# Kernel tuning notes

Measured on AMD Instinct MI355X. Metric: run time of the kernel, lower is better.

Reference implementation:

```python
import jax, jax.numpy as jnp
import numpy as np

# Module hyperparameters (from init_kwargs)
H, F = 8, 32            # num_heads, attention_filters
RY, RX = 3, 3           # spatial_radius
PH, PW = 2 * RY + 1, 2 * RX + 1
S = PH * PW             # patch_size = 49
HF = H * F


def setup_inputs() -> dict:
    key = jax.random.key(0)
    ks = jax.random.split(key, 6)
    B, Y, X, C = 4, 64, 64, 256
    x = jax.random.normal(ks[0], (B, Y, X, C), jnp.float32)
    # 1x1 conv kernels == dense matrices over the channel dim (no bias)
    Wq = jax.random.normal(ks[1], (C, HF), jnp.float32) / np.sqrt(C)
    Wk = jax.random.normal(ks[2], (C, HF), jnp.float32) / np.sqrt(C)
    Wv = jax.random.normal(ks[3], (C, HF), jnp.float32) / np.sqrt(C)
    Wo = jax.random.normal(ks[4], (HF, C), jnp.float32) / np.sqrt(HF)
    pos_emb = jax.random.normal(ks[5], (S, HF), jnp.float32) * 0.02
    return {"x": x, "Wq": Wq, "Wk": Wk, "Wv": Wv, "Wo": Wo, "pos_emb": pos_emb}


def reference(x, Wq, Wk, Wv, Wo, pos_emb):
    B, Y, X, C = x.shape
    dtype = x.dtype
    # 1x1 conv projections
    Q = x @ Wq                       # (B,Y,X,HF)
    K = x @ Wk
    V = x @ Wv
    # clipped patch centers (borders reuse interior patches)
    cy = jnp.clip(jnp.arange(Y), RY, Y - RY - 1)   # (Y,)
    cx = jnp.clip(jnp.arange(X), RX, X - RX - 1)   # (X,)
    # query relative-position indices within its patch
    qy = jnp.arange(Y) - cy + RY
    qx = jnp.arange(X) - cx + RX
    qidx = qy[:, None] * PW + qx[None, :]          # (Y,X) in [0,S)
    Q = Q + pos_emb[qidx]                          # add query pos embedding (HF)
    Q = Q.reshape(B, Y, X, H, F)
    K = K.reshape(B, Y, X, H, F)
    V = V.reshape(B, Y, X, H, F)
    cy_g, cx_g = jnp.meshgrid(cy, cx, indexing="ij")  # (Y,X)
    scale = jnp.asarray(1.0 / np.sqrt(F), dtype)
    NEG = jnp.asarray(-1e9, dtype)
    m = jnp.full((B, Y, X, H, 1), NEG, dtype)      # running max
    l = jnp.zeros((B, Y, X, H, 1), dtype)          # running sum-exp
    acc = jnp.zeros((B, Y, X, H, F), dtype)        # running value accumulator
    dy_vec = np.arange(-RY, RY + 1)                # within-chunk offsets ('col' mode)
    for dx in range(-RX, RX + 1):                  # chunk loop over columns (7 chunks)
        ny = jnp.clip(cy_g[None, :, :] + dy_vec[:, None, None], 0, Y - 1)  # (PH,Y,X)
        nx = jnp.clip(cx_g[None, :, :] + dx, 0, X - 1)                     # (1,Y,X)
        nx = jnp.broadcast_to(nx, ny.shape)
        sidx = (dy_vec + RY) * PW + (dx + RX)      # (PH,) relative-pos indices
        # gather neighbor K/V: (B,PH,Y,X,H,F)
        Kc = K[:, ny, nx] + pos_emb[sidx].reshape(PH, 1, 1, H, F)
        Vc = V[:, ny, nx]
        sc = jnp.einsum("byxhf,bsyxhf->byxhs", Q, Kc) * scale  # (B,Y,X,H,PH)
        new_m = jnp.maximum(m, sc.max(axis=-1, keepdims=True))
        alpha = jnp.exp(m - new_m)
        p = jnp.exp(sc - new_m)
        l = l * alpha + p.sum(axis=-1, keepdims=True)
        acc = acc * alpha + jnp.einsum("byxhs,bsyxhf->byxhf", p, Vc)
        m = new_m
    out = (acc / (l + 1e-8)).reshape(B, Y, X, HF) @ Wo
    return out
```

## Files before the change

kernel.cpp:

```cpp
#include <hip/hip_runtime.h>
#include <hip/hip_bf16.h>

static constexpr int NPOS = 4 * 64 * 64;
static constexpr int CD   = 256;
#define QSCALE (0.17677669529663687f * 1.4426950408889634f)

typedef __attribute__((ext_vector_type(8))) short bf16x8;
typedef __attribute__((ext_vector_type(4))) float f32x4;

__device__ __forceinline__ unsigned short bfbits(float f) {
    union { __hip_bfloat16 h; unsigned short u; } cv;
    cv.h = __float2bfloat16(f);
    return cv.u;
}
__device__ __forceinline__ unsigned int packbf2(float lo, float hi) {
    union { __hip_bfloat162 h; unsigned int u; } cv;
    cv.h.x = __float2bfloat16(lo);
    cv.h.y = __float2bfloat16(hi);
    return cv.u;
}
__device__ __forceinline__ uint4 pack8(float4 a, float4 b) {
    uint4 u;
    u.x = packbf2(a.x, a.y); u.y = packbf2(a.z, a.w);
    u.z = packbf2(b.x, b.y); u.w = packbf2(b.z, b.w);
    return u;
}
template<int CTRL>
__device__ __forceinline__ float dpp_mov(float v) {
    return __int_as_float(
        __builtin_amdgcn_update_dpp(0, __float_as_int(v), CTRL, 0xF, 0xF, true));
}
template<int IMM>
__device__ __forceinline__ float swz(float v) {
    return __int_as_float(__builtin_amdgcn_ds_swizzle(__float_as_int(v), IMM));
}
__device__ __forceinline__ void async16(void* lds, const void* g) {
    __builtin_amdgcn_global_load_lds(
        (const __attribute__((address_space(1))) unsigned int*)g,
        (__attribute__((address_space(3))) unsigned int*)lds, 16, 0, 0);
}

__global__ __launch_bounds__(256) void convert_kernel(
    const float* __restrict__ Wq, const float* __restrict__ Wk,
    const float* __restrict__ Wv, const float* __restrict__ Wo,
    const float* __restrict__ pe,
    __hip_bfloat16* __restrict__ Wfrag,
    __hip_bfloat16* __restrict__ pebf,
    __hip_bfloat16* __restrict__ Wofrag)
{
    int t = blockIdx.x * 256 + threadIdx.x;
    if (t < 24576) {
        int L = t & 63, ng = (t >> 6) & 7, s = (t >> 9) & 7, T = t >> 12;
        int mat = T >> 1;
        const float* src = (mat == 0) ? Wq : (mat == 1) ? Wk : Wv;
        int ncol  = (T & 1) * 128 + ng * 16 + (L & 15);
        int kbase = s * 32 + (L >> 4) * 8;
        __hip_bfloat16* dst = Wfrag + ((size_t)((T * 8 + s) * 8 + ng) * 64 + L) * 8;
#pragma unroll
        for (int j = 0; j < 8; ++j)
            dst[j] = __float2bfloat16(src[(kbase + j) * 256 + ncol]);
    } else if (t < 26624) {
        int u = t - 24576;
        int L = u & 63, Tn = (u >> 6) & 3, h = u >> 8;
        int s = Tn * 16 + (L & 15);
        int kbase = (L >> 4) * 8;
        __hip_bfloat16* dst = pebf + ((size_t)((h * 4 + Tn) * 64 + L)) * 8;
#pragma unroll
        for (int j = 0; j < 8; ++j) {
            float v = (s < 49) ? pe[s * 256 + h * 32 + kbase + j] * QSCALE : 0.f;
            dst[j] = __float2bfloat16(v);
        }
    } else if (t < 34816) {
        int u = t - 26624;
        int L = u & 63, ng = (u >> 6) & 7, s = (u >> 9) & 7, T = (u >> 12) & 1;
        int ncol  = T * 128 + ng * 16 + (L & 15);
        int kbase = s * 32 + (L >> 4) * 8;
        __hip_bfloat16* dst = Wofrag + ((size_t)((T * 8 + s) * 8 + ng) * 64 + L) * 8;
#pragma unroll
        for (int j = 0; j < 8; ++j)
            dst[j] = __float2bfloat16(Wo[(kbase + j) * 256 + ncol]);
    }
}

__global__ __launch_bounds__(256, 4) void qkv_mfma(
    const float* __restrict__ x,
    const __hip_bfloat16* __restrict__ Wfrag,
    const float* __restrict__ pe,
    unsigned short* __restrict__ QA,
    unsigned short* __restrict__ Kd,
    unsigned short* __restrict__ Vt)
{
    __shared__ __align__(16) unsigned short smem[256 * 68];
    short* As0 = (short*)smem;
    short* As1 = As0 + 2048;
    const int t = threadIdx.x;
    const int rowbase = blockIdx.x * 64;
    const int g = blockIdx.y;
    const int L = t & 63;
    const int wave = t >> 6;
    const int quad = L >> 4, lrow = L & 15;
    const int T = g * 2 + (wave >> 1);
    const int ngb = (wave & 1) * 4;

    f32x4 acc[4][4];
#pragma unroll
    for (int i = 0; i < 4; ++i)
#pragma unroll
        for (int j = 0; j < 4; ++j) acc[i][j] = (f32x4){0.f, 0.f, 0.f, 0.f};

    const float* xsrc = x + (size_t)(rowbase + (t >> 2)) * CD + (t & 3) * 8;

    float4 f0 = ((const float4*)xsrc)[0];
    float4 f1 = ((const float4*)xsrc)[1];
    ((uint4*)As0)[t] = pack8(f0, f1);
    f0 = ((const float4*)(xsrc + 32))[0];
    f1 = ((const float4*)(xsrc + 32))[1];
    __syncthreads();

#pragma unroll
    for (int s = 0; s < 8; ++s) {
        bf16x8 bfr[4];
#pragma unroll
        for (int j = 0; j < 4; ++j)
            bfr[j] = *(const bf16x8*)(Wfrag +
                      ((size_t)((T * 8 + s) * 8 + ngb + j) * 64 + L) * 8);
        if (s < 7) {
            ((uint4*)((s & 1) ? As0 : As1))[t] = pack8(f0, f1);
            if (s < 6) {
                f0 = ((const float4*)(xsrc + (s + 2) * 32))[0];
                f1 = ((const float4*)(xsrc + (s + 2) * 32))[1];
            }
        }
        const short* Ab = (s & 1) ? As1 : As0;
#pragma unroll
        for (int i = 0; i < 4; ++i) {
            bf16x8 af = *(const bf16x8*)(Ab + (i * 16 + lrow) * 32 + quad * 8);
#pragma unroll
            for (int j = 0; j < 4; ++j)
                acc[i][j] = __builtin_amdgcn_mfma_f32_16x16x32_bf16(af, bfr[j], acc[i][j], 0, 0, 0);
        }
        __syncthreads();
    }

    if (g == 0) {
#pragma unroll
        for (int i = 0; i < 4; ++i)
#pragma unroll
            for (int r = 0; r < 4; ++r) {
                int row = rowbase + i * 16 + quad * 4 + r;
                int yy = (row >> 6) & 63, xx = row & 63;
                int cy = min(max(yy, 3), 60), cx = min(max(xx, 3), 60);
                int qidx = (yy - cy + 3) * 7 + (xx - cx + 3);
#pragma unroll
                for (int j = 0; j < 4; ++j) {
                    int c = wave * 64 + j * 16 + lrow;
                    QA[(size_t)row * CD + c] = bfbits(acc[i][j][r] + pe[qidx * 256 + c]);
                }
            }
    } else if (g == 1) {
#pragma unroll
        for (int i = 0; i < 4; ++i)
#pragma unroll
            for (int r = 0; r < 4; ++r) {
                int row = rowbase + i * 16 + quad * 4 + r;
#pragma unroll
                for (int j = 0; j < 4; ++j) {
                    int c = wave * 64 + j * 16 + lrow;
                    Kd[(size_t)row * CD + c] = bfbits(acc[i][j][r] * QSCALE);
                }
            }
    } else {
        unsigned short* vt = smem;
#pragma unroll
        for (int i = 0; i < 4; ++i)
#pragma unroll
            for (int j = 0; j < 4; ++j) {
                int c = wave * 64 + j * 16 + lrow;
                int row0 = i * 16 + quad * 4;
                *(unsigned int*)&vt[c * 68 + row0] =
                    (unsigned int)bfbits(acc[i][j][0]) | ((unsigned int)bfbits(acc[i][j][1]) << 16);
                *(unsigned int*)&vt[c * 68 + row0 + 2] =
                    (unsigned int)bfbits(acc[i][j][2]) | ((unsigned int)bfbits(acc[i][j][3]) << 16);
            }
        __syncthreads();
        const int grp = t >> 4, lig = t & 15;
        const int row_off = lig * 4;
#pragma unroll
        for (int pass = 0; pass < 16; ++pass) {
            int c = pass * 16 + grp;
            *(ushort4*)(Vt + (size_t)c * 16384 + rowbase + row_off) =
                *(const ushort4*)&vt[c * 68 + row_off];
        }
    }
}

__global__ __launch_bounds__(256) void attn_mfma(
    unsigned short* QA,
    const unsigned short* __restrict__ Kd,
    const unsigned short* __restrict__ Vt,
    const __hip_bfloat16* __restrict__ pebf)
{
    __shared__ float qpes[4][16 * 64];
    __shared__ __align__(16) unsigned short ps[4][16 * 40];
    const int t = threadIdx.x, w = t >> 6, L = t & 63;
    const int lrow = L & 15, quad = L >> 4;
    const int id = blockIdx.x * 4 + w;
    const int tile = id >> 3, h = id & 7;
    const int pos0 = tile * 16;
    const int x0 = pos0 & 63;
    const int yy = (pos0 >> 6) & 63, bb = pos0 >> 12;
    const int cy = min(max(yy, 3), 60);

    int cxr[4];
#pragma unroll
    for (int r = 0; r < 4; ++r)
        cxr[r] = min(max(x0 + quad * 4 + r, 3), 60) - x0 + 5;

    const int kc0 = min(max(x0 - 8 + lrow, 0), 63);
    const int kc1 = min(max(x0 + 8 + lrow, 0), 63);

    const bf16x8 qa = *(const bf16x8*)(QA + (size_t)(pos0 + lrow) * 256 + h * 32 + quad * 8);

    float* qp = qpes[w];
    const f32x4 zero = {0.f, 0.f, 0.f, 0.f};
#pragma unroll
    for (int Tn = 0; Tn < 4; ++Tn) {
        bf16x8 bp = *(const bf16x8*)(pebf + ((size_t)((h * 4 + Tn) * 64 + L)) * 8);
        f32x4 c = __builtin_amdgcn_mfma_f32_16x16x32_bf16(qa, bp, zero, 0, 0, 0);
#pragma unroll
        for (int r = 0; r < 4; ++r)
            qp[(quad * 4 + r) * 64 + Tn * 16 + lrow] = c[r];
    }
    __builtin_amdgcn_s_waitcnt(0xc07f);

    float lacc[4] = {0.f, 0.f, 0.f, 0.f};
    f32x4 o0 = zero, o1 = zero;
    unsigned short* pw = ps[w];
    int rowpos = bb * 4096 + (cy - 3) * 64;

    const size_t koff = h * 32 + quad * 8;
    const size_t voff0 = (size_t)(h * 32 + lrow) * 16384 + x0 - 8 + quad * 8;
    const size_t voff1 = (size_t)(h * 32 + 16 + lrow) * 16384 + x0 - 8 + quad * 8;
    bf16x8 bk0 = *(const bf16x8*)(Kd + (size_t)(rowpos + kc0) * 256 + koff);
    bf16x8 bk1 = *(const bf16x8*)(Kd + (size_t)(rowpos + kc1) * 256 + koff);
    bf16x8 bv0 = *(const bf16x8*)(Vt + voff0 + rowpos);
    bf16x8 bv1 = *(const bf16x8*)(Vt + voff1 + rowpos);

    for (int dy = 0; dy < 7; ++dy) {
        const int rnext = rowpos + 64;
        bf16x8 nk0, nk1, nv0, nv1;
        if (dy < 6) {
            nk0 = *(const bf16x8*)(Kd + (size_t)(rnext + kc0) * 256 + koff);
            nk1 = *(const bf16x8*)(Kd + (size_t)(rnext + kc1) * 256 + koff);
            nv0 = *(const bf16x8*)(Vt + voff0 + rnext);
            nv1 = *(const bf16x8*)(Vt + voff1 + rnext);
        }
        f32x4 sc0 = __builtin_amdgcn_mfma_f32_16x16x32_bf16(qa, bk0, zero, 0, 0, 0);
        f32x4 sc1 = __builtin_amdgcn_mfma_f32_16x16x32_bf16(qa, bk1, zero, 0, 0, 0);
        const int dy7 = dy * 7;
#pragma unroll
        for (int r = 0; r < 4; ++r) {
            const int i = quad * 4 + r;
            {
                int dx3 = lrow - cxr[r];
                float qpe = qp[i * 64 + dy7 + min(max(dx3, 0), 6)];
                float e = exp2f(sc0[r] + qpe);
                float p = ((unsigned)dx3 <= 6u) ? e : 0.f;
                lacc[r] += p;
                pw[i * 40 + lrow] = bfbits(p);
            }
            {
                int dx3 = 16 + lrow - cxr[r];
                float qpe = qp[i * 64 + dy7 + min(max(dx3, 0), 6)];
                float e = exp2f(sc1[r] + qpe);
                float p = ((unsigned)dx3 <= 6u) ? e : 0.f;
                lacc[r] += p;
                pw[i * 40 + 16 + lrow] = bfbits(p);
            }
        }
        __builtin_amdgcn_s_waitcnt(0xc07f);
        const bf16x8 pa = *(const bf16x8*)(pw + lrow * 40 + quad * 8);
        o0 = __builtin_amdgcn_mfma_f32_16x16x32_bf16(pa, bv0, o0, 0, 0, 0);
        o1 = __builtin_amdgcn_mfma_f32_16x16x32_bf16(pa, bv1, o1, 0, 0, 0);
        bk0 = nk0; bk1 = nk1; bv0 = nv0; bv1 = nv1;
        rowpos = rnext;
    }

#pragma unroll
    for (int r = 0; r < 4; ++r) {
        float v = lacc[r];
        v += dpp_mov<0xB1>(v);
        v += dpp_mov<0x4E>(v);
        v += swz<0x101F>(v);
        v += swz<0x201F>(v);
        const float inv = 1.f / (v + 1e-8f);
        const int row = pos0 + quad * 4 + r;
        QA[(size_t)row * 256 + h * 32 + lrow]      = bfbits(o0[r] * inv);
        QA[(size_t)row * 256 + h * 32 + 16 + lrow] = bfbits(o1[r] * inv);
    }
}

__global__ __launch_bounds__(256, 4) void oproj_mfma(
    const unsigned short* __restrict__ A,
    const __hip_bfloat16* __restrict__ Wofrag,
    float* __restrict__ out)
{
    __shared__ __align__(16) short As[2][32 * 32];
    const int t = threadIdx.x;
    const int rowbase = blockIdx.x * 32;
    const int L = t & 63;
    const int wave = t >> 6;
    const int quad = L >> 4, lrow = L & 15;
    const int T = wave >> 1;
    const int ngb = (wave & 1) * 4;

    f32x4 acc[2][4];
#pragma unroll
    for (int i = 0; i < 2; ++i)
#pragma unroll
        for (int j = 0; j < 4; ++j) acc[i][j] = (f32x4){0.f, 0.f, 0.f, 0.f};

    const unsigned short* asrc = A + (size_t)(rowbase + (t >> 2)) * CD + (t & 3) * 8;
    short* d0 = &As[0][t * 8];
    short* d1 = &As[1][t * 8];

    if (t < 128) async16(d0, asrc);
    __syncthreads();

#pragma unroll
    for (int s = 0; s < 8; ++s) {
        if (s < 7 && t < 128) async16((s & 1) ? d0 : d1, asrc + (s + 1) * 32);
        bf16x8 bfr[4];
#pragma unroll
        for (int j = 0; j < 4; ++j)
            bfr[j] = *(const bf16x8*)(Wofrag +
                      ((size_t)((T * 8 + s) * 8 + ngb + j) * 64 + L) * 8);
        const short* Ab = As[s & 1];
#pragma unroll
        for (int i = 0; i < 2; ++i) {
            bf16x8 af = *(const bf16x8*)(Ab + (i * 16 + lrow) * 32 + quad * 8);
#pragma unroll
            for (int j = 0; j < 4; ++j)
                acc[i][j] = __builtin_amdgcn_mfma_f32_16x16x32_bf16(af, bfr[j], acc[i][j], 0, 0, 0);
        }
        __syncthreads();
    }

#pragma unroll
    for (int i = 0; i < 2; ++i)
#pragma unroll
        for (int r = 0; r < 4; ++r) {
            int row = rowbase + i * 16 + quad * 4 + r;
#pragma unroll
            for (int j = 0; j < 4; ++j) {
                int c = wave * 64 + j * 16 + lrow;
                out[(size_t)row * CD + c] = acc[i][j][r];
            }
        }
}

extern "C" void kernel_launch(void* const* d_in, const int* in_sizes, int n_in,
                              void* d_out, int out_size, void* d_ws, size_t ws_size,
                              hipStream_t stream)
{
    const float* x  = (const float*)d_in[0];
    const float* Wq = (const float*)d_in[1];
    const float* Wk = (const float*)d_in[2];
    const float* Wv = (const float*)d_in[3];
    const float* Wo = (const float*)d_in[4];
    const float* pe = (const float*)d_in[5];
    float* out = (float*)d_out;

    char* ws = (char*)d_ws;
    unsigned short* QA = (unsigned short*)ws;
    unsigned short* Kd = (unsigned short*)(ws + (8u << 20));
    unsigned short* Vt = (unsigned short*)(ws + (16u << 20));
    char* fr = ws + (24u << 20) + 4096;
    __hip_bfloat16* Wfrag  = (__hip_bfloat16*)fr;
    __hip_bfloat16* pebf   = (__hip_bfloat16*)(fr + (384u << 10));
    __hip_bfloat16* Wofrag = (__hip_bfloat16*)(fr + (416u << 10));

    convert_kernel<<<136, 256, 0, stream>>>(Wq, Wk, Wv, Wo, pe, Wfrag, pebf, Wofrag);
    qkv_mfma<<<dim3(256, 3), 256, 0, stream>>>(x, Wfrag, pe, QA, Kd, Vt);
    attn_mfma<<<2048, 256, 0, stream>>>(QA, Kd, Vt, pebf);
    oproj_mfma<<<512, 256, 0, stream>>>(QA, Wofrag, out);
}
```

Before: 128.6 us.

## Fuse attention and output projection into one kernel via LDS staging

Merges the attention kernel and the output-projection GEMM into one kernel. Each block now handles one 16-position tile across all 8 heads, with each wave processing two heads. The normalized attention output is staged in shared memory and immediately multiplied by Wo, so the bf16 intermediate no longer round-trips through global memory and one launch disappears. In exchange, the block count halves, per-wave work is serialized over two heads, and each block re-reads all of Wo.

```diff
diff --git a/kernel.cpp b/kernel.cpp
--- a/kernel.cpp
+++ b/kernel.cpp
@@ -33,11 +33,6 @@
 template<int IMM>
 __device__ __forceinline__ float swz(float v) {
     return __int_as_float(__builtin_amdgcn_ds_swizzle(__float_as_int(v), IMM));
-}
-__device__ __forceinline__ void async16(void* lds, const void* g) {
-    __builtin_amdgcn_global_load_lds(
-        (const __attribute__((address_space(1))) unsigned int*)g,
-        (__attribute__((address_space(3))) unsigned int*)lds, 16, 0, 0);
 }
 
 __global__ __launch_bounds__(256) void convert_kernel(
@@ -194,19 +189,20 @@
     }
 }
 
-__global__ __launch_bounds__(256) void attn_mfma(
-    unsigned short* QA,
+__global__ __launch_bounds__(256) void attn_oproj(
+    const unsigned short* __restrict__ QA,
     const unsigned short* __restrict__ Kd,
     const unsigned short* __restrict__ Vt,
-    const __hip_bfloat16* __restrict__ pebf)
+    const __hip_bfloat16* __restrict__ pebf,
+    const __hip_bfloat16* __restrict__ Wofrag,
+    float* __restrict__ out)
 {
     __shared__ float qpes[4][16 * 64];
     __shared__ __align__(16) unsigned short ps[4][16 * 40];
+    __shared__ __align__(16) unsigned short At[16 * 264];
     const int t = threadIdx.x, w = t >> 6, L = t & 63;
     const int lrow = L & 15, quad = L >> 4;
-    const int id = blockIdx.x * 4 + w;
-    const int tile = id >> 3, h = id & 7;
-    const int pos0 = tile * 16;
+    const int pos0 = blockIdx.x * 16;
     const int x0 = pos0 & 63;
     const int yy = (pos0 >> 6) & 63, bb = pos0 >> 12;
     const int cy = min(max(yy, 3), 60);
@@ -218,145 +214,121 @@
 
     const int kc0 = min(max(x0 - 8 + lrow, 0), 63);
     const int kc1 = min(max(x0 + 8 + lrow, 0), 63);
-
-    const bf16x8 qa = *(const bf16x8*)(QA + (size_t)(pos0 + lrow) * 256 + h * 32 + quad * 8);
-
+    const f32x4 zero = {0.f, 0.f, 0.f, 0.f};
     float* qp = qpes[w];
-    const f32x4 zero = {0.f, 0.f, 0.f, 0.f};
-#pragma unroll
-    for (int Tn = 0; Tn < 4; ++Tn) {
-        bf16x8 bp = *(const bf16x8*)(pebf + ((size_t)((h * 4 + Tn) * 64 + L)) * 8);
-        f32x4 c = __builtin_amdgcn_mfma_f32_16x16x32_bf16(qa, bp, zero, 0, 0, 0);
-#pragma unroll
-        for (int r = 0; r < 4; ++r)
-            qp[(quad * 4 + r) * 64 + Tn * 16 + lrow] = c[r];
-    }
-    __builtin_amdgcn_s_waitcnt(0xc07f);
-
-    float lacc[4] = {0.f, 0.f, 0.f, 0.f};
-    f32x4 o0 = zero, o1 = zero;
     unsigned short* pw = ps[w];
-    int rowpos = bb * 4096 + (cy - 3) * 64;
-
-    const size_t koff = h * 32 + quad * 8;
-    const size_t voff0 = (size_t)(h * 32 + lrow) * 16384 + x0 - 8 + quad * 8;
-    const size_t voff1 = (size_t)(h * 32 + 16 + lrow) * 16384 + x0 - 8 + quad * 8;
-    bf16x8 bk0 = *(const bf16x8*)(Kd + (size_t)(rowpos + kc0) * 256 + koff);
-    bf16x8 bk1 = *(const bf16x8*)(Kd + (size_t)(rowpos + kc1) * 256 + koff);
-    bf16x8 bv0 = *(const bf16x8*)(Vt + voff0 + rowpos);
-    bf16x8 bv1 = *(const bf16x8*)(Vt + voff1 + rowpos);
-
-    for (int dy = 0; dy < 7; ++dy) {
-        const int rnext = rowpos + 64;
-        bf16x8 nk0, nk1, nv0, nv1;
-        if (dy < 6) {
-            nk0 = *(const bf16x8*)(Kd + (size_t)(rnext + kc0) * 256 + koff);
-            nk1 = *(const bf16x8*)(Kd + (size_t)(rnext + kc1) * 256 + koff);
-            nv0 = *(const bf16x8*)(Vt + voff0 + rnext);
-            nv1 = *(const bf16x8*)(Vt + voff1 + rnext);
-        }
-        f32x4 sc0 = __builtin_amdgcn_mfma_f32_16x16x32_bf16(qa, bk0, zero, 0, 0, 0);
-        f32x4 sc1 = __builtin_amdgcn_mfma_f32_16x16x32_bf16(qa, bk1, zero, 0, 0, 0);
-        const int dy7 = dy * 7;
+
+#pragma unroll
+    for (int u = 0; u < 2; ++u) {
+        const int h = w + u * 4;
+
+        const bf16x8 qa = *(const bf16x8*)(QA + (size_t)(pos0 + lrow) * 256 + h * 32 + quad * 8);
+
+#pragma unroll
+        for (int Tn = 0; Tn < 4; ++Tn) {
+            bf16x8 bp = *(const bf16x8*)(pebf + ((size_t)((h * 4 + Tn) * 64 + L)) * 8);
+            f32x4 c = __builtin_amdgcn_mfma_f32_16x16x32_bf16(qa, bp, zero, 0, 0, 0);
+#pragma unroll
+            for (int r = 0; r < 4; ++r)
+                qp[(quad * 4 + r) * 64 + Tn * 16 + lrow] = c[r];
+        }
+        __builtin_amdgcn_s_waitcnt(0xc07f);
+
+        float lacc[4] = {0.f, 0.f, 0.f, 0.f};
+        f32x4 o0 = zero, o1 = zero;
+        int rowpos = bb * 4096 + (cy - 3) * 64;
+
+        const size_t koff = h * 32 + quad * 8;
+        const size_t voff0 = (size_t)(h * 32 + lrow) * 16384 + x0 - 8 + quad * 8;
+        const size_t voff1 = (size_t)(h * 32 + 16 + lrow) * 16384 + x0 - 8 + quad * 8;
+        bf16x8 bk0 = *(const bf16x8*)(Kd + (size_t)(rowpos + kc0) * 256 + koff);
+        bf16x8 bk1 = *(const bf16x8*)(Kd + (size_t)(rowpos + kc1) * 256 + koff);
+        bf16x8 bv0 = *(const bf16x8*)(Vt + voff0 + rowpos);
+        bf16x8 bv1 = *(const bf16x8*)(Vt + voff1 + rowpos);
+
+        for (int dy = 0; dy < 7; ++dy) {
+            const int rnext = rowpos + 64;
+            bf16x8 nk0, nk1, nv0, nv1;
+            if (dy < 6) {
+                nk0 = *(const bf16x8*)(Kd + (size_t)(rnext + kc0) * 256 + koff);
+                nk1 = *(const bf16x8*)(Kd + (size_t)(rnext + kc1) * 256 + koff);
+                nv0 = *(const bf16x8*)(Vt + voff0 + rnext);
+                nv1 = *(const bf16x8*)(Vt + voff1 + rnext);
+            }
+            f32x4 sc0 = __builtin_amdgcn_mfma_f32_16x16x32_bf16(qa, bk0, zero, 0, 0, 0);
+            f32x4 sc1 = __builtin_amdgcn_mfma_f32_16x16x32_bf16(qa, bk1, zero, 0, 0, 0);
+            const int dy7 = dy * 7;
+#pragma unroll
+            for (int r = 0; r < 4; ++r) {
+                const int i = quad * 4 + r;
+                {
+                    int dx3 = lrow - cxr[r];
+                    float qpe = qp[i * 64 + dy7 + min(max(dx3, 0), 6)];
+                    float e = exp2f(sc0[r] + qpe);
+                    float p = ((unsigned)dx3 <= 6u) ? e : 0.f;
+                    lacc[r] += p;
+                    pw[i * 40 + lrow] = bfbits(p);
+                }
+                {
+                    int dx3 = 16 + lrow - cxr[r];
+                    float qpe = qp[i * 64 + dy7 + min(max(dx3, 0), 6)];
+                    float e = exp2f(sc1[r] + qpe);
+                    float p = ((unsigned)dx3 <= 6u) ? e : 0.f;
+                    lacc[r] += p;
+                    pw[i * 40 + 16 + lrow] = bfbits(p);
+                }
+            }
+            __builtin_amdgcn_s_waitcnt(0xc07f);
+            const bf16x8 pa = *(const bf16x8*)(pw + lrow * 40 + quad * 8);
+            o0 = __builtin_amdgcn_mfma_f32_16x16x32_bf16(pa, bv0, o0, 0, 0, 0);
+            o1 = __builtin_amdgcn_mfma_f32_16x16x32_bf16(pa, bv1, o1, 0, 0, 0);
+            bk0 = nk0; bk1 = nk1; bv0 = nv0; bv1 = nv1;
+            rowpos = rnext;
+        }
+
 #pragma unroll
         for (int r = 0; r < 4; ++r) {
-            const int i = quad * 4 + r;
-            {
-                int dx3 = lrow - cxr[r];
-                float qpe = qp[i * 64 + dy7 + min(max(dx3, 0), 6)];
-                float e = exp2f(sc0[r] + qpe);
-                float p = ((unsigned)dx3 <= 6u) ? e : 0.f;
-                lacc[r] += p;
-                pw[i * 40 + lrow] = bfbits(p);
-            }
-            {
-                int dx3 = 16 + lrow - cxr[r];
-                float qpe = qp[i * 64 + dy7 + min(max(dx3, 0), 6)];
-                float e = exp2f(sc1[r] + qpe);
-                float p = ((unsigned)dx3 <= 6u) ? e : 0.f;
-                lacc[r] += p;
-                pw[i * 40 + 16 + lrow] = bfbits(p);
-            }
-        }
-        __builtin_amdgcn_s_waitcnt(0xc07f);
-        const bf16x8 pa = *(const bf16x8*)(pw + lrow * 40 + quad * 8);
-        o0 = __builtin_amdgcn_mfma_f32_16x16x32_bf16(pa, bv0, o0, 0, 0, 0);
-        o1 = __builtin_amdgcn_mfma_f32_16x16x32_bf16(pa, bv1, o1, 0, 0, 0);
-        bk0 = nk0; bk1 = nk1; bv0 = nv0; bv1 = nv1;
-        rowpos = rnext;
-    }
-
-#pragma unroll
-    for (int r = 0; r < 4; ++r) {
-        float v = lacc[r];
-        v += dpp_mov<0xB1>(v);
-        v += dpp_mov<0x4E>(v);
-        v += swz<0x101F>(v);
-        v += swz<0x201F>(v);
-        const float inv = 1.f / (v + 1e-8f);
-        const int row = pos0 + quad * 4 + r;
-        QA[(size_t)row * 256 + h * 32 + lrow]      = bfbits(o0[r] * inv);
-        QA[(size_t)row * 256 + h * 32 + 16 + lrow] = bfbits(o1[r] * inv);
-    }
-}
-
-__global__ __launch_bounds__(256, 4) void oproj_mfma(
-    const unsigned short* __restrict__ A,
-    const __hip_bfloat16* __restrict__ Wofrag,
-    float* __restrict__ out)
-{
-    __shared__ __align__(16) short As[2][32 * 32];
-    const int t = threadIdx.x;
-    const int rowbase = blockIdx.x * 32;
-    const int L = t & 63;
-    const int wave = t >> 6;
-    const int quad = L >> 4, lrow = L & 15;
-    const int T = wave >> 1;
-    const int ngb = (wave & 1) * 4;
-
-    f32x4 acc[2][4];
-#pragma unroll
-    for (int i = 0; i < 2; ++i)
-#pragma unroll
-        for (int j = 0; j < 4; ++j) acc[i][j] = (f32x4){0.f, 0.f, 0.f, 0.f};
-
-    const unsigned short* asrc = A + (size_t)(rowbase + (t >> 2)) * CD + (t & 3) * 8;
-    short* d0 = &As[0][t * 8];
-    short* d1 = &As[1][t * 8];
-
-    if (t < 128) async16(d0, asrc);
+            float v = lacc[r];
+            v += dpp_mov<0xB1>(v);
+            v += dpp_mov<0x4E>(v);
+            v += swz<0x101F>(v);
+            v += swz<0x201F>(v);
+            const float inv = 1.f / (v + 1e-8f);
+            const int arow = quad * 4 + r;
+            At[arow * 264 + h * 32 + lrow]      = bfbits(o0[r] * inv);
+            At[arow * 264 + h * 32 + 16 + lrow] = bfbits(o1[r] * inv);
+        }
+    }
     __syncthreads();
 
+    const int T = w >> 1;
+    const int ngb = (w & 1) * 4;
+    f32x4 acc[4];
+#pragma unroll
+    for (int j = 0; j < 4; ++j) acc[j] = zero;
+
 #pragma unroll
     for (int s = 0; s < 8; ++s) {
-        if (s < 7 && t < 128) async16((s & 1) ? d0 : d1, asrc + (s + 1) * 32);
         bf16x8 bfr[4];
 #pragma unroll
         for (int j = 0; j < 4; ++j)
             bfr[j] = *(const bf16x8*)(Wofrag +
                       ((size_t)((T * 8 + s) * 8 + ngb + j) * 64 + L) * 8);
-        const short* Ab = As[s & 1];
-#pragma unroll
-        for (int i = 0; i < 2; ++i) {
-            bf16x8 af = *(const bf16x8*)(Ab + (i * 16 + lrow) * 32 + quad * 8);
-#pragma unroll
-            for (int j = 0; j < 4; ++j)
-                acc[i][j] = __builtin_amdgcn_mfma_f32_16x16x32_bf16(af, bfr[j], acc[i][j], 0, 0, 0);
-        }
-        __syncthreads();
-    }
-
-#pragma unroll
-    for (int i = 0; i < 2; ++i)
-#pragma unroll
-        for (int r = 0; r < 4; ++r) {
-            int row = rowbase + i * 16 + quad * 4 + r;
-#pragma unroll
-            for (int j = 0; j < 4; ++j) {
-                int c = wave * 64 + j * 16 + lrow;
-                out[(size_t)row * CD + c] = acc[i][j][r];
-            }
-        }
+        bf16x8 af = *(const bf16x8*)(At + lrow * 264 + s * 32 + quad * 8);
+#pragma unroll
+        for (int j = 0; j < 4; ++j)
+            acc[j] = __builtin_amdgcn_mfma_f32_16x16x32_bf16(af, bfr[j], acc[j], 0, 0, 0);
+    }
+
+#pragma unroll
+    for (int r = 0; r < 4; ++r) {
+        int row = pos0 + quad * 4 + r;
+#pragma unroll
+        for (int j = 0; j < 4; ++j) {
+            int c = w * 64 + j * 16 + lrow;
+            out[(size_t)row * CD + c] = acc[j][r];
+        }
+    }
 }
 
 extern "C" void kernel_launch(void* const* d_in, const int* in_sizes, int n_in,
@@ -382,6 +354,5 @@
 
     convert_kernel<<<136, 256, 0, stream>>>(Wq, Wk, Wv, Wo, pe, Wfrag, pebf, Wofrag);
     qkv_mfma<<<dim3(256, 3), 256, 0, stream>>>(x, Wfrag, pe, QA, Kd, Vt);
-    attn_mfma<<<2048, 256, 0, stream>>>(QA, Kd, Vt, pebf);
-    oproj_mfma<<<512, 256, 0, stream>>>(QA, Wofrag, out);
-}
+    attn_oproj<<<1024, 256, 0, stream>>>(QA, Kd, Vt, pebf, Wofrag, out);
+}
```

After: 130.6 us. About the same (+1.5%).
